# Kernel optimization log

Hardware: AMD Instinct MI355X
Metric: run time of the kernel (lower is better)

Reference implementation:

```python
import jax, jax.numpy as jnp
import numpy as np
from jax import lax

NEG_SLOPE = 0.2
BN_EPS = 1e-5


def _edges(n_nodes, n_total):
    # complete graph (no self loops) on the first n_nodes nodes, as in create_complete_graph,
    # plus PyG GATConv default add_self_loops over ALL n_total nodes.
    i = np.arange(n_nodes)
    src = np.repeat(i, n_nodes)
    dst = np.tile(i, n_nodes)
    keep = src != dst
    loops = np.arange(n_total)
    src = np.concatenate([src[keep], loops]).astype(np.int32)
    dst = np.concatenate([dst[keep], loops]).astype(np.int32)
    return jnp.asarray(src), jnp.asarray(dst)


def _bn_eval(x, g, b, m, v):
    # x: [B, C, H, W]; eval-mode batchnorm with running stats
    inv = g / jnp.sqrt(v + BN_EPS)
    return x * inv[None, :, None, None] + (b - m * inv)[None, :, None, None]


def _gat(x, W, a_src, a_dst, bias, src, dst, n_total):
    h = x @ W                      # [N, D_out]
    s = h @ a_src                  # [N] per-node source score
    d = h @ a_dst                  # [N] per-node dest score
    e = jax.nn.leaky_relu(s[src] + d[dst], NEG_SLOPE)          # [E]
    emax = jax.ops.segment_max(e, dst, num_segments=n_total)   # [N]
    ex = jnp.exp(e - emax[dst])
    denom = jax.ops.segment_sum(ex, dst, num_segments=n_total)
    alpha = ex / denom[dst]                                    # [E]
    out = jax.ops.segment_sum(alpha[:, None] * h[src], dst, num_segments=n_total)
    return out + bias


def setup_inputs() -> dict:
    key = jax.random.key(0)
    ks = jax.random.split(key, 12)
    B, H, W = 8, 64, 64

    def rn(k, shape, s):
        return jax.random.normal(k, shape, jnp.float32) * s

    return {
        "images": jax.random.normal(ks[0], (B, 3, H, W), jnp.float32),
        "conv1_w": rn(ks[1], (64, 3, 3, 3), 0.1), "conv1_b": jnp.zeros((64,), jnp.float32),
        "bn1_g": jnp.ones((64,), jnp.float32), "bn1_b": jnp.zeros((64,), jnp.float32),
        "bn1_m": jnp.zeros((64,), jnp.float32), "bn1_v": jnp.ones((64,), jnp.float32),
        "conv2_w": rn(ks[2], (128, 64, 3, 3), 0.05), "conv2_b": jnp.zeros((128,), jnp.float32),
        "bn2_g": jnp.ones((128,), jnp.float32), "bn2_b": jnp.zeros((128,), jnp.float32),
        "bn2_m": jnp.zeros((128,), jnp.float32), "bn2_v": jnp.ones((128,), jnp.float32),
        "gat1_w": rn(ks[3], (128, 256), 0.05), "gat1_asrc": rn(ks[4], (256,), 0.05),
        "gat1_adst": rn(ks[5], (256,), 0.05), "gat1_bias": jnp.zeros((256,), jnp.float32),
        "gat2_w": rn(ks[6], (256, 128), 0.05), "gat2_asrc": rn(ks[7], (128,), 0.05),
        "gat2_adst": rn(ks[8], (128,), 0.05), "gat2_bias": jnp.zeros((128,), jnp.float32),
        "out_w": rn(ks[9], (128, 10), 0.05), "out_b": jnp.zeros((10,), jnp.float32),
    }


def reference(images, conv1_w, conv1_b, bn1_g, bn1_b, bn1_m, bn1_v,
              conv2_w, conv2_b, bn2_g, bn2_b, bn2_m, bn2_v,
              gat1_w, gat1_asrc, gat1_adst, gat1_bias,
              gat2_w, gat2_asrc, gat2_adst, gat2_bias,
              out_w, out_b):
    dn = ("NCHW", "OIHW", "NCHW")
    x = lax.conv_general_dilated(images, conv1_w, (1, 1), "SAME", dimension_numbers=dn)
    x = x + conv1_b[None, :, None, None]
    x = jax.nn.relu(_bn_eval(x, bn1_g, bn1_b, bn1_m, bn1_v))
    x = lax.reduce_window(x, -jnp.inf, lax.max, (1, 1, 2, 2), (1, 1, 2, 2), "VALID")
    x = lax.conv_general_dilated(x, conv2_w, (1, 1), "SAME", dimension_numbers=dn)
    x = x + conv2_b[None, :, None, None]
    x = jax.nn.relu(_bn_eval(x, bn2_g, bn2_b, bn2_m, bn2_v))

    B = x.shape[0]
    n_nodes = x.shape[2] * x.shape[3]          # (H/2)*(W/2) = 1024
    x = x.reshape(B, 128, n_nodes).transpose(0, 2, 1).reshape(-1, 128)  # [B*n, 128]
    n_total = B * n_nodes
    src, dst = _edges(n_nodes, n_total)

    x = jax.nn.relu(_gat(x, gat1_w, gat1_asrc, gat1_adst, gat1_bias, src, dst, n_total))
    x = jax.nn.relu(_gat(x, gat2_w, gat2_asrc, gat2_adst, gat2_bias, src, dst, n_total))

    x = x.reshape(B, n_nodes, 128).mean(axis=1)   # global_mean_pool over each image's nodes
    logits = x @ out_w + out_b
    return jax.nn.log_softmax(logits, axis=1)
```

## Files before the change

kernel.cpp:

```cpp
#include <hip/hip_runtime.h>
#include <math.h>

#define BN_EPS 1e-5f
#define NEG_SLOPE 0.2f

__device__ __forceinline__ float relu_f(float x) { return x > 0.f ? x : 0.f; }
__device__ __forceinline__ float leaky_f(float z) { return z > 0.f ? z : NEG_SLOPE * z; }

__global__ void conv1_pool(const float* __restrict__ img, const float* __restrict__ w,
                           const float* __restrict__ cb, const float* __restrict__ g,
                           const float* __restrict__ bb, const float* __restrict__ m,
                           const float* __restrict__ vv, float* __restrict__ out)
{
    int blk = blockIdx.x;
    int q = blk & 3, cog = (blk >> 2) & 15, b = blk >> 6;
    int t = threadIdx.x;
    int x = t & 31, y = (q << 3) + (t >> 5);

    float acc[4][4] = {};
#pragma unroll
    for (int ci = 0; ci < 3; ++ci) {
        const float* ib = img + (b * 3 + ci) * 4096;
        float rv[4][4];
#pragma unroll
        for (int r = 0; r < 4; ++r) {
            int yy = 2 * y - 1 + r;
            bool yok = (unsigned)yy < 64u;
            const float* p = ib + yy * 64 + 2 * x;
            float2 c01 = yok ? *(const float2*)p : make_float2(0.f, 0.f);
            rv[r][1] = c01.x;
            rv[r][2] = c01.y;
            rv[r][0] = (yok && x > 0) ? p[-1] : 0.f;
            rv[r][3] = (yok && x < 31) ? p[2] : 0.f;
        }
#pragma unroll
        for (int j = 0; j < 4; ++j) {
            const float* wj = w + ((cog * 4 + j) * 3 + ci) * 9;
#pragma unroll
            for (int ky = 0; ky < 3; ++ky)
#pragma unroll
                for (int kx = 0; kx < 3; ++kx) {
                    float wvv = wj[ky * 3 + kx];
#pragma unroll
                    for (int py = 0; py < 2; ++py)
#pragma unroll
                        for (int px = 0; px < 2; ++px)
                            acc[j][py * 2 + px] += rv[py + ky][px + kx] * wvv;
                }
        }
    }
#pragma unroll
    for (int j = 0; j < 4; ++j) {
        int co = cog * 4 + j;
        float inv = g[co] / sqrtf(vv[co] + BN_EPS);
        float sh = cb[co] * inv + (bb[co] - m[co] * inv);
        float v0 = relu_f(acc[j][0] * inv + sh);
        float v1 = relu_f(acc[j][1] * inv + sh);
        float v2 = relu_f(acc[j][2] * inv + sh);
        float v3 = relu_f(acc[j][3] * inv + sh);
        out[((b * 64 + co) * 32 + y) * 32 + x] = fmaxf(fmaxf(v0, v1), fmaxf(v2, v3));
    }
}

__global__ void conv2_split(const float* __restrict__ in, const float* __restrict__ w,
                            float* __restrict__ pacc01, float* __restrict__ pacc23)
{
    int blk = blockIdx.x;
    int kz = blk & 3, half = (blk >> 2) & 1, cog = (blk >> 3) & 31, b = blk >> 8;
    int t = threadIdx.x;
    int x2p = (t & 15) * 2;
    int y = half * 16 + (t >> 4);
    bool xnz = x2p != 0;
    bool xhi = x2p == 30;
    const float* ibase = in + b * 64 * 1024 + kz * 16 * 1024;
    int xb = xnz ? x2p - 1 : 0;

    float acc[4][2] = {};

#pragma unroll 2
    for (int ci = 0; ci < 16; ++ci) {
        const float* cb2 = ibase + ci * 1024;
        float rc[3][4];
#pragma unroll
        for (int r = 0; r < 3; ++r) {
            int yy = y - 1 + r;
            bool yok = (unsigned)yy < 32u;
            const float* p = cb2 + yy * 32 + xb;
            float4 f = yok ? *(const float4*)p : make_float4(0.f, 0.f, 0.f, 0.f);
            rc[r][0] = xnz ? f.x : 0.f;
            rc[r][1] = xnz ? f.y : f.x;
            rc[r][2] = xnz ? f.z : f.y;
            float r3 = xnz ? f.w : f.z;
            rc[r][3] = xhi ? 0.f : r3;
        }
#pragma unroll
        for (int j = 0; j < 4; ++j) {
            const float* wj = w + ((cog * 4 + j) * 64 + kz * 16 + ci) * 9;
#pragma unroll
            for (int ky = 0; ky < 3; ++ky)
#pragma unroll
                for (int kx = 0; kx < 3; ++kx) {
                    float wvv = wj[ky * 3 + kx];
                    acc[j][0] += rc[ky][kx] * wvv;
                    acc[j][1] += rc[ky][kx + 1] * wvv;
                }
        }
    }

    float* pp = (kz & 2 ? pacc23 : pacc01) + (size_t)(kz & 1) * 1048576;
    int bid = b * 64 + cog * 2 + half;
    size_t base = ((size_t)bid * 256 + t) * 8;
    float4 s0 = {acc[0][0], acc[1][0], acc[2][0], acc[3][0]};
    float4 s1 = {acc[0][1], acc[1][1], acc[2][1], acc[3][1]};
    *(float4*)&pp[base] = s0;
    *(float4*)&pp[base + 4] = s1;
}

__global__ void conv2_combine(const float* __restrict__ p01, const float* __restrict__ p23,
                              const float* __restrict__ cb, const float* __restrict__ g,
                              const float* __restrict__ bb, const float* __restrict__ m,
                              const float* __restrict__ vv, float* __restrict__ x0)
{
    int gid = blockIdx.x * 256 + threadIdx.x;
    int t = gid & 255, bid = gid >> 8;
    int half = bid & 1, cog = (bid >> 1) & 31, b = bid >> 6;
    size_t off = (size_t)gid * 8;

    float4 s0 = {0.f, 0.f, 0.f, 0.f}, s1 = {0.f, 0.f, 0.f, 0.f};
    const float* pl0 = p01;
    const float* pl1 = p01 + 1048576;
    const float* pl2 = p23;
    const float* pl3 = p23 + 1048576;
#pragma unroll
    for (int kz = 0; kz < 4; ++kz) {
        const float* pp = kz == 0 ? pl0 : kz == 1 ? pl1 : kz == 2 ? pl2 : pl3;
        float4 u0 = *(const float4*)&pp[off];
        float4 u1 = *(const float4*)&pp[off + 4];
        s0.x += u0.x; s0.y += u0.y; s0.z += u0.z; s0.w += u0.w;
        s1.x += u1.x; s1.y += u1.y; s1.z += u1.z; s1.w += u1.w;
    }

    float4 gg = ((const float4*)g)[cog];
    float4 vvv = ((const float4*)vv)[cog];
    float4 bbb = ((const float4*)bb)[cog];
    float4 mm = ((const float4*)m)[cog];
    float4 cbb = ((const float4*)cb)[cog];
    float ix = gg.x / sqrtf(vvv.x + BN_EPS);
    float iy = gg.y / sqrtf(vvv.y + BN_EPS);
    float iz = gg.z / sqrtf(vvv.z + BN_EPS);
    float iw = gg.w / sqrtf(vvv.w + BN_EPS);
    float shx = cbb.x * ix + (bbb.x - mm.x * ix);
    float shy = cbb.y * iy + (bbb.y - mm.y * iy);
    float shz = cbb.z * iz + (bbb.z - mm.z * iz);
    float shw = cbb.w * iw + (bbb.w - mm.w * iw);

    float4 o0 = {relu_f(s0.x * ix + shx), relu_f(s0.y * iy + shy),
                 relu_f(s0.z * iz + shz), relu_f(s0.w * iw + shw)};
    float4 o1 = {relu_f(s1.x * ix + shx), relu_f(s1.y * iy + shy),
                 relu_f(s1.z * iz + shz), relu_f(s1.w * iw + shw)};

    int y = half * 16 + (t >> 4), x2p = (t & 15) * 2;
    int n0 = b * 1024 + y * 32 + x2p;
    *(float4*)&x0[(size_t)n0 * 128 + cog * 4] = o0;
    *(float4*)&x0[(size_t)(n0 + 1) * 128 + cog * 4] = o1;
}

template <int K, int N, bool SELF, bool SCORE>
__global__ void gemm32(const float* __restrict__ A, const float* __restrict__ Ahi,
                       const float* __restrict__ abias,
                       const float* __restrict__ B, float* __restrict__ C,
                       const float* __restrict__ asrc, const float* __restrict__ adst,
                       float* __restrict__ sp, float* __restrict__ dp)
{
    __shared__ float As[16][32];
    __shared__ float Bs[16][64];
    int t = threadIdx.x;
    int m0 = blockIdx.x * 32;
    int n0 = blockIdx.y * 64;
    int tx = t & 15, ty = t >> 4;
    int am = t >> 2, akq = (t & 3) * 4;
    bool hi = SELF && m0 >= 1024;
    const float* Ab = hi ? Ahi : A;
    float acc[4][4] = {};

    for (int k0 = 0; k0 < K; k0 += 16) {
        float4 av = *(const float4*)&Ab[(size_t)(m0 + am) * K + k0 + akq];
        if (hi) {
            float4 bz = *(const float4*)&abias[k0 + akq];
            av.x = relu_f(av.x + bz.x);
            av.y = relu_f(av.y + bz.y);
            av.z = relu_f(av.z + bz.z);
            av.w = relu_f(av.w + bz.w);
        }
        float4 bv0 = *(const float4*)&B[(size_t)(k0 + ty) * N + n0 + tx * 4];
        float4 bv1 = *(const float4*)&B[(size_t)(k0 + 8 + ty) * N + n0 + tx * 4];
        __syncthreads();
        As[akq + 0][am] = av.x;
        As[akq + 1][am] = av.y;
        As[akq + 2][am] = av.z;
        As[akq + 3][am] = av.w;
        *(float4*)&Bs[ty][tx * 4] = bv0;
        *(float4*)&Bs[ty + 8][tx * 4] = bv1;
        __syncthreads();
#pragma unroll
        for (int kk = 0; kk < 16; ++kk) {
            float4 a4 = *(const float4*)&As[kk][ty * 4];
            float4 b4 = *(const float4*)&Bs[kk][tx * 4];
            float aa[4] = {a4.x, a4.y, a4.z, a4.w};
            float bb4[4] = {b4.x, b4.y, b4.z, b4.w};
#pragma unroll
            for (int i = 0; i < 4; ++i)
#pragma unroll
                for (int j = 0; j < 4; ++j)
                    acc[i][j] += aa[i] * bb4[j];
        }
    }
#pragma unroll
    for (int i = 0; i < 4; ++i) {
        float4 o = {acc[i][0], acc[i][1], acc[i][2], acc[i][3]};
        *(float4*)&C[(size_t)(m0 + ty * 4 + i) * N + n0 + tx * 4] = o;
    }

    if (SCORE && m0 < 1024) {
        float4 as4 = *(const float4*)&asrc[n0 + tx * 4];
        float4 ad4 = *(const float4*)&adst[n0 + tx * 4];
#pragma unroll
        for (int i = 0; i < 4; ++i) {
            float ss = acc[i][0] * as4.x + acc[i][1] * as4.y +
                       acc[i][2] * as4.z + acc[i][3] * as4.w;
            float dd = acc[i][0] * ad4.x + acc[i][1] * ad4.y +
                       acc[i][2] * ad4.z + acc[i][3] * ad4.w;
#pragma unroll
            for (int off = 1; off < 16; off <<= 1) {
                ss += __shfl_xor(ss, off);
                dd += __shfl_xor(dd, off);
            }
            if (tx == 0) {
                sp[blockIdx.y * 1024 + m0 + ty * 4 + i] = ss;
                dp[blockIdx.y * 1024 + m0 + ty * 4 + i] = dd;
            }
        }
    }
}

template <int D, int KS, int NT>
__global__ void gat_agg_gemm(const float* __restrict__ h, const float* __restrict__ sp,
                             const float* __restrict__ dp, float* __restrict__ pacc,
                             float* __restrict__ pden)
{
    __shared__ float Ss[1024];
    __shared__ float As[16][32];
    __shared__ float Bs[16][64];
    __shared__ float red[2];
    __shared__ float part[16][32];

    const int CH = 1024 / KS;
    int t = threadIdx.x;
    int m0 = blockIdx.x * 32;
    int n0 = blockIdx.y * 64;
    int kz = blockIdx.z;
    int tx = t & 15, ty = t >> 4;
    int ug = t >> 3, vg4 = (t & 7) * 4;

    float4 sa = {0.f, 0.f, 0.f, 0.f}, sb = {0.f, 0.f, 0.f, 0.f};
#pragma unroll
    for (int nt = 0; nt < NT; ++nt) {
        float4 u = *(const float4*)&sp[nt * 1024 + t * 8];
        float4 v = *(const float4*)&sp[nt * 1024 + t * 8 + 4];
        sa.x += u.x; sa.y += u.y; sa.z += u.z; sa.w += u.w;
        sb.x += v.x; sb.y += v.y; sb.z += v.z; sb.w += v.w;
    }
    *(float4*)&Ss[t * 8] = sa;
    *(float4*)&Ss[t * 8 + 4] = sb;
    float lm = fmaxf(fmaxf(fmaxf(sa.x, sa.y), fmaxf(sa.z, sa.w)),
                     fmaxf(fmaxf(sb.x, sb.y), fmaxf(sb.z, sb.w)));
#pragma unroll
    for (int off = 1; off < 64; off <<= 1) lm = fmaxf(lm, __shfl_xor(lm, off));
    if ((t & 63) == 0) red[t >> 6] = lm;
    __syncthreads();
    float smax = fmaxf(red[0], red[1]);

    float4 dv = {0.f, 0.f, 0.f, 0.f};
#pragma unroll
    for (int nt = 0; nt < NT; ++nt) {
        float4 u = *(const float4*)&dp[nt * 1024 + m0 + vg4];
        dv.x += u.x; dv.y += u.y; dv.z += u.z; dv.w += u.w;
    }
    float4 mv = {leaky_f(smax + dv.x), leaky_f(smax + dv.y),
                 leaky_f(smax + dv.z), leaky_f(smax + dv.w)};
    float4 dsum = {0.f, 0.f, 0.f, 0.f};
    float acc[4][4] = {};

    for (int k0 = kz * CH; k0 < kz * CH + CH; k0 += 16) {
        float4 bv0 = *(const float4*)&h[(size_t)(k0 + ty) * D + n0 + tx * 4];
        float4 bv1 = *(const float4*)&h[(size_t)(k0 + 8 + ty) * D + n0 + tx * 4];
        float su = Ss[k0 + ug];
        float4 avv;
        avv.x = __expf(leaky_f(su + dv.x) - mv.x);
        avv.y = __expf(leaky_f(su + dv.y) - mv.y);
        avv.z = __expf(leaky_f(su + dv.z) - mv.z);
        avv.w = __expf(leaky_f(su + dv.w) - mv.w);
        dsum.x += avv.x; dsum.y += avv.y; dsum.z += avv.z; dsum.w += avv.w;
        __syncthreads();
        *(float4*)&As[ug][vg4] = avv;
        *(float4*)&Bs[ty][tx * 4] = bv0;
        *(float4*)&Bs[ty + 8][tx * 4] = bv1;
        __syncthreads();
#pragma unroll
        for (int kk = 0; kk < 16; ++kk) {
            float4 a4 = *(const float4*)&As[kk][ty * 4];
            float4 b4 = *(const float4*)&Bs[kk][tx * 4];
            float aa[4] = {a4.x, a4.y, a4.z, a4.w};
            float bb4[4] = {b4.x, b4.y, b4.z, b4.w};
#pragma unroll
            for (int i = 0; i < 4; ++i)
#pragma unroll
                for (int j = 0; j < 4; ++j)
                    acc[i][j] += aa[i] * bb4[j];
        }
    }

    __syncthreads();
    *(float4*)&part[ug][vg4] = dsum;
    __syncthreads();

#pragma unroll
    for (int i = 0; i < 4; ++i) {
        int r = ty * 4 + i;
        float4 o = {acc[i][0], acc[i][1], acc[i][2], acc[i][3]};
        *(float4*)&pacc[((size_t)kz * 1024 + m0 + r) * D + n0 + tx * 4] = o;
    }
    if (t < 32) {
        float den = 0.f;
#pragma unroll
        for (int u = 0; u < 16; ++u) den += part[u][t];
        pden[kz * 1024 + m0 + t] = den;
    }
}

template <int D, int KS>
__global__ void gat_combine(const float* __restrict__ pacc, const float* __restrict__ pden,
                            const float* __restrict__ bias, float* __restrict__ out)
{
    int idx = blockIdx.x * blockDim.x + threadIdx.x;
    if (idx >= 1024 * D / 4) return;
    int c4 = idx & (D / 4 - 1);
    int v = idx / (D / 4);
    float4 a = {0.f, 0.f, 0.f, 0.f};
    float den = 0.f;
#pragma unroll
    for (int ks = 0; ks < KS; ++ks) {
        float4 p = ((const float4*)pacc)[(size_t)(ks * 1024 + v) * (D / 4) + c4];
        a.x += p.x; a.y += p.y; a.z += p.z; a.w += p.w;
        den += pden[ks * 1024 + v];
    }
    float rd = 1.f / den;
    float4 bz = ((const float4*)bias)[c4];
    float4 o = {relu_f(a.x * rd + bz.x), relu_f(a.y * rd + bz.y),
                relu_f(a.z * rd + bz.z), relu_f(a.w * rd + bz.w)};
    ((float4*)out)[(size_t)v * (D / 4) + c4] = o;
}

__global__ void pool_part(const float* __restrict__ x2, const float* __restrict__ h2,
                          const float* __restrict__ bias2, float* __restrict__ part)
{
    int b = blockIdx.x >> 4, seg = blockIdx.x & 15, t = threadIdx.x;
    float acc = 0.f;
    if (b == 0) {
        const float* p = x2 + ((size_t)seg * 64) * 128 + t;
#pragma unroll 8
        for (int n = 0; n < 64; ++n) acc += p[(size_t)n * 128];
    } else {
        float bz = bias2[t];
        const float* p = h2 + ((size_t)b * 1024 + seg * 64) * 128 + t;
#pragma unroll 8
        for (int n = 0; n < 64; ++n) acc += relu_f(p[(size_t)n * 128] + bz);
    }
    part[(b * 16 + seg) * 128 + t] = acc;
}

__global__ void head_kernel(const float* __restrict__ part, const float* __restrict__ ow,
                            const float* __restrict__ ob, float* __restrict__ out)
{
    __shared__ float pooled[128];
    __shared__ float logits[10];
    int b = blockIdx.x, t = threadIdx.x;
    float acc = 0.f;
#pragma unroll
    for (int sgi = 0; sgi < 16; ++sgi) acc += part[(b * 16 + sgi) * 128 + t];
    pooled[t] = acc * (1.f / 1024.f);
    __syncthreads();
    if (t < 10) {
        float l = ob[t];
        for (int c = 0; c < 128; ++c) l += pooled[c] * ow[c * 10 + t];
        logits[t] = l;
    }
    __syncthreads();
    if (t == 0) {
        float mx = logits[0];
        for (int j = 1; j < 10; ++j) mx = fmaxf(mx, logits[j]);
        float sum = 0.f;
        for (int j = 0; j < 10; ++j) sum += expf(logits[j] - mx);
        float lse = mx + logf(sum);
        for (int j = 0; j < 10; ++j) out[b * 10 + j] = logits[j] - lse;
    }
}

extern "C" void kernel_launch(void* const* d_in, const int* in_sizes, int n_in,
                              void* d_out, int out_size, void* d_ws, size_t ws_size,
                              hipStream_t stream)
{
    const float* images = (const float*)d_in[0];
    const float* c1w = (const float*)d_in[1];
    const float* c1b = (const float*)d_in[2];
    const float* bn1g = (const float*)d_in[3];
    const float* bn1b = (const float*)d_in[4];
    const float* bn1m = (const float*)d_in[5];
    const float* bn1v = (const float*)d_in[6];
    const float* c2w = (const float*)d_in[7];
    const float* c2b = (const float*)d_in[8];
    const float* bn2g = (const float*)d_in[9];
    const float* bn2b = (const float*)d_in[10];
    const float* bn2m = (const float*)d_in[11];
    const float* bn2v = (const float*)d_in[12];
    const float* g1w = (const float*)d_in[13];
    const float* g1as = (const float*)d_in[14];
    const float* g1ad = (const float*)d_in[15];
    const float* g1b = (const float*)d_in[16];
    const float* g2w = (const float*)d_in[17];
    const float* g2as = (const float*)d_in[18];
    const float* g2ad = (const float*)d_in[19];
    const float* g2b = (const float*)d_in[20];
    const float* ow = (const float*)d_in[21];
    const float* ob = (const float*)d_in[22];
    float* out = (float*)d_out;

    float* ws = (float*)d_ws;
    float* x1    = ws;
    float* bufc1 = ws + 2097152;
    float* h1    = ws + 2621440;
    float* x0    = ws + 4718592;
    float* h2    = ws + 5767168;
    float* sp1   = ws + 6815744;
    float* dp1   = ws + 6819840;
    float* sp2   = ws + 6823936;
    float* dp2   = ws + 6825984;
    float* part  = bufc1;
    float* pden1 = bufc1 + 16384;
    float* pden2 = bufc1 + 24576;
    float* pacc1 = x0;
    float* pacc2 = h1;
    float* x2    = x0;
    float* c2p01 = x1;
    float* c2p23 = h1;

    conv1_pool<<<512, 256, 0, stream>>>(images, c1w, c1b, bn1g, bn1b, bn1m, bn1v, bufc1);
    conv2_split<<<2048, 256, 0, stream>>>(bufc1, c2w, c2p01, c2p23);
    conv2_combine<<<512, 256, 0, stream>>>(c2p01, c2p23, c2b, bn2g, bn2b, bn2m, bn2v, x0);

    gemm32<128, 256, false, true><<<dim3(256, 4), 128, 0, stream>>>(
        x0, x0, nullptr, g1w, h1, g1as, g1ad, sp1, dp1);
    gat_agg_gemm<256, 8, 4><<<dim3(32, 4, 8), 128, 0, stream>>>(h1, sp1, dp1, pacc1, pden1);
    gat_combine<256, 8><<<256, 256, 0, stream>>>(pacc1, pden1, g1b, x1);

    gemm32<256, 128, true, true><<<dim3(256, 2), 128, 0, stream>>>(
        x1, h1, g1b, g2w, h2, g2as, g2ad, sp2, dp2);
    gat_agg_gemm<128, 16, 2><<<dim3(32, 2, 16), 128, 0, stream>>>(h2, sp2, dp2, pacc2, pden2);
    gat_combine<128, 16><<<128, 256, 0, stream>>>(pacc2, pden2, g2b, x2);

    pool_part<<<128, 128, 0, stream>>>(x2, h2, g2b, part);
    head_kernel<<<8, 128, 0, stream>>>(part, ow, ob, out);
}
```

Baseline: 204.3 us.

## Halve conv2 K-split and use 256-thread GEMM/aggregation blocks with 2x4 microtiles

The conv2 input-channel split drops from 4 to 2 partial slices. This halves the partial-sum traffic and simplifies the combine step to two reads, at the cost of fewer blocks, each doing more serial work. The gemm32 and gat_agg_gemm kernels move from 128 threads with 4x4 per-thread tiles to 256 threads with 2x4 tiles, and the A smem tile is padded to 33 columns. This raises the thread count per block and lowers register pressure, but each thread now reuses fewer values from shared memory per load.

```diff
diff --git a/kernel.cpp b/kernel.cpp
--- a/kernel.cpp
+++ b/kernel.cpp
@@ -63,22 +63,22 @@
 }
 
 __global__ void conv2_split(const float* __restrict__ in, const float* __restrict__ w,
-                            float* __restrict__ pacc01, float* __restrict__ pacc23)
+                            float* __restrict__ c2p)
 {
     int blk = blockIdx.x;
-    int kz = blk & 3, half = (blk >> 2) & 1, cog = (blk >> 3) & 31, b = blk >> 8;
+    int kz = blk & 1, half = (blk >> 1) & 1, cog = (blk >> 2) & 31, b = blk >> 7;
     int t = threadIdx.x;
     int x2p = (t & 15) * 2;
     int y = half * 16 + (t >> 4);
     bool xnz = x2p != 0;
     bool xhi = x2p == 30;
-    const float* ibase = in + b * 64 * 1024 + kz * 16 * 1024;
+    const float* ibase = in + b * 65536 + kz * 32768;
     int xb = xnz ? x2p - 1 : 0;
 
     float acc[4][2] = {};
 
 #pragma unroll 2
-    for (int ci = 0; ci < 16; ++ci) {
+    for (int ci = 0; ci < 32; ++ci) {
         const float* cb2 = ibase + ci * 1024;
         float rc[3][4];
 #pragma unroll
@@ -95,7 +95,7 @@
         }
 #pragma unroll
         for (int j = 0; j < 4; ++j) {
-            const float* wj = w + ((cog * 4 + j) * 64 + kz * 16 + ci) * 9;
+            const float* wj = w + ((cog * 4 + j) * 64 + kz * 32 + ci) * 9;
 #pragma unroll
             for (int ky = 0; ky < 3; ++ky)
 #pragma unroll
@@ -107,7 +107,7 @@
         }
     }
 
-    float* pp = (kz & 2 ? pacc23 : pacc01) + (size_t)(kz & 1) * 1048576;
+    float* pp = c2p + (size_t)kz * 1048576;
     int bid = b * 64 + cog * 2 + half;
     size_t base = ((size_t)bid * 256 + t) * 8;
     float4 s0 = {acc[0][0], acc[1][0], acc[2][0], acc[3][0]};
@@ -116,7 +116,7 @@
     *(float4*)&pp[base + 4] = s1;
 }
 
-__global__ void conv2_combine(const float* __restrict__ p01, const float* __restrict__ p23,
+__global__ void conv2_combine(const float* __restrict__ c2p,
                               const float* __restrict__ cb, const float* __restrict__ g,
                               const float* __restrict__ bb, const float* __restrict__ m,
                               const float* __restrict__ vv, float* __restrict__ x0)
@@ -126,19 +126,12 @@
     int half = bid & 1, cog = (bid >> 1) & 31, b = bid >> 6;
     size_t off = (size_t)gid * 8;
 
-    float4 s0 = {0.f, 0.f, 0.f, 0.f}, s1 = {0.f, 0.f, 0.f, 0.f};
-    const float* pl0 = p01;
-    const float* pl1 = p01 + 1048576;
-    const float* pl2 = p23;
-    const float* pl3 = p23 + 1048576;
-#pragma unroll
-    for (int kz = 0; kz < 4; ++kz) {
-        const float* pp = kz == 0 ? pl0 : kz == 1 ? pl1 : kz == 2 ? pl2 : pl3;
-        float4 u0 = *(const float4*)&pp[off];
-        float4 u1 = *(const float4*)&pp[off + 4];
-        s0.x += u0.x; s0.y += u0.y; s0.z += u0.z; s0.w += u0.w;
-        s1.x += u1.x; s1.y += u1.y; s1.z += u1.z; s1.w += u1.w;
-    }
+    float4 u0 = *(const float4*)&c2p[off];
+    float4 u1 = *(const float4*)&c2p[off + 4];
+    float4 w0 = *(const float4*)&c2p[1048576 + off];
+    float4 w1 = *(const float4*)&c2p[1048576 + off + 4];
+    float sx = u0.x + w0.x, sy = u0.y + w0.y, sz = u0.z + w0.z, sw = u0.w + w0.w;
+    float qx = u1.x + w1.x, qy = u1.y + w1.y, qz = u1.z + w1.z, qw = u1.w + w1.w;
 
     float4 gg = ((const float4*)g)[cog];
     float4 vvv = ((const float4*)vv)[cog];
@@ -154,10 +147,10 @@
     float shz = cbb.z * iz + (bbb.z - mm.z * iz);
     float shw = cbb.w * iw + (bbb.w - mm.w * iw);
 
-    float4 o0 = {relu_f(s0.x * ix + shx), relu_f(s0.y * iy + shy),
-                 relu_f(s0.z * iz + shz), relu_f(s0.w * iw + shw)};
-    float4 o1 = {relu_f(s1.x * ix + shx), relu_f(s1.y * iy + shy),
-                 relu_f(s1.z * iz + shz), relu_f(s1.w * iw + shw)};
+    float4 o0 = {relu_f(sx * ix + shx), relu_f(sy * iy + shy),
+                 relu_f(sz * iz + shz), relu_f(sw * iw + shw)};
+    float4 o1 = {relu_f(qx * ix + shx), relu_f(qy * iy + shy),
+                 relu_f(qz * iz + shz), relu_f(qw * iw + shw)};
 
     int y = half * 16 + (t >> 4), x2p = (t & 15) * 2;
     int n0 = b * 1024 + y * 32 + x2p;
@@ -172,60 +165,50 @@
                        const float* __restrict__ asrc, const float* __restrict__ adst,
                        float* __restrict__ sp, float* __restrict__ dp)
 {
-    __shared__ float As[16][32];
+    __shared__ float As[16][33];
     __shared__ float Bs[16][64];
     int t = threadIdx.x;
     int m0 = blockIdx.x * 32;
     int n0 = blockIdx.y * 64;
     int tx = t & 15, ty = t >> 4;
-    int am = t >> 2, akq = (t & 3) * 4;
+    int am = t >> 3, ak2 = (t & 7) * 2;
     bool hi = SELF && m0 >= 1024;
     const float* Ab = hi ? Ahi : A;
-    float acc[4][4] = {};
+    float acc[2][4] = {};
 
     for (int k0 = 0; k0 < K; k0 += 16) {
-        float4 av = *(const float4*)&Ab[(size_t)(m0 + am) * K + k0 + akq];
+        float2 av = *(const float2*)&Ab[(size_t)(m0 + am) * K + k0 + ak2];
         if (hi) {
-            float4 bz = *(const float4*)&abias[k0 + akq];
-            av.x = relu_f(av.x + bz.x);
-            av.y = relu_f(av.y + bz.y);
-            av.z = relu_f(av.z + bz.z);
-            av.w = relu_f(av.w + bz.w);
-        }
-        float4 bv0 = *(const float4*)&B[(size_t)(k0 + ty) * N + n0 + tx * 4];
-        float4 bv1 = *(const float4*)&B[(size_t)(k0 + 8 + ty) * N + n0 + tx * 4];
+            av.x = relu_f(av.x + abias[k0 + ak2]);
+            av.y = relu_f(av.y + abias[k0 + ak2 + 1]);
+        }
+        float4 bv = *(const float4*)&B[(size_t)(k0 + ty) * N + n0 + tx * 4];
         __syncthreads();
-        As[akq + 0][am] = av.x;
-        As[akq + 1][am] = av.y;
-        As[akq + 2][am] = av.z;
-        As[akq + 3][am] = av.w;
-        *(float4*)&Bs[ty][tx * 4] = bv0;
-        *(float4*)&Bs[ty + 8][tx * 4] = bv1;
+        As[ak2][am] = av.x;
+        As[ak2 + 1][am] = av.y;
+        *(float4*)&Bs[ty][tx * 4] = bv;
         __syncthreads();
 #pragma unroll
         for (int kk = 0; kk < 16; ++kk) {
-            float4 a4 = *(const float4*)&As[kk][ty * 4];
+            float a0 = As[kk][ty * 2], a1 = As[kk][ty * 2 + 1];
             float4 b4 = *(const float4*)&Bs[kk][tx * 4];
-            float aa[4] = {a4.x, a4.y, a4.z, a4.w};
-            float bb4[4] = {b4.x, b4.y, b4.z, b4.w};
-#pragma unroll
-            for (int i = 0; i < 4; ++i)
-#pragma unroll
-                for (int j = 0; j < 4; ++j)
-                    acc[i][j] += aa[i] * bb4[j];
-        }
-    }
-#pragma unroll
-    for (int i = 0; i < 4; ++i) {
+            acc[0][0] += a0 * b4.x; acc[0][1] += a0 * b4.y;
+            acc[0][2] += a0 * b4.z; acc[0][3] += a0 * b4.w;
+            acc[1][0] += a1 * b4.x; acc[1][1] += a1 * b4.y;
+            acc[1][2] += a1 * b4.z; acc[1][3] += a1 * b4.w;
+        }
+    }
+#pragma unroll
+    for (int i = 0; i < 2; ++i) {
         float4 o = {acc[i][0], acc[i][1], acc[i][2], acc[i][3]};
-        *(float4*)&C[(size_t)(m0 + ty * 4 + i) * N + n0 + tx * 4] = o;
+        *(float4*)&C[(size_t)(m0 + ty * 2 + i) * N + n0 + tx * 4] = o;
     }
 
     if (SCORE && m0 < 1024) {
         float4 as4 = *(const float4*)&asrc[n0 + tx * 4];
         float4 ad4 = *(const float4*)&adst[n0 + tx * 4];
 #pragma unroll
-        for (int i = 0; i < 4; ++i) {
+        for (int i = 0; i < 2; ++i) {
             float ss = acc[i][0] * as4.x + acc[i][1] * as4.y +
                        acc[i][2] * as4.z + acc[i][3] * as4.w;
             float dd = acc[i][0] * ad4.x + acc[i][1] * ad4.y +
@@ -236,8 +219,8 @@
                 dd += __shfl_xor(dd, off);
             }
             if (tx == 0) {
-                sp[blockIdx.y * 1024 + m0 + ty * 4 + i] = ss;
-                dp[blockIdx.y * 1024 + m0 + ty * 4 + i] = dd;
+                sp[blockIdx.y * 1024 + m0 + ty * 2 + i] = ss;
+                dp[blockIdx.y * 1024 + m0 + ty * 2 + i] = dd;
             }
         }
     }
@@ -249,9 +232,9 @@
                              float* __restrict__ pden)
 {
     __shared__ float Ss[1024];
-    __shared__ float As[16][32];
+    __shared__ float As[16][33];
     __shared__ float Bs[16][64];
-    __shared__ float red[2];
+    __shared__ float red[4];
     __shared__ float part[16][32];
 
     const int CH = 1024 / KS;
@@ -260,75 +243,63 @@
     int n0 = blockIdx.y * 64;
     int kz = blockIdx.z;
     int tx = t & 15, ty = t >> 4;
-    int ug = t >> 3, vg4 = (t & 7) * 4;
-
-    float4 sa = {0.f, 0.f, 0.f, 0.f}, sb = {0.f, 0.f, 0.f, 0.f};
+    int vg2 = tx * 2;
+
+    float4 sa = {0.f, 0.f, 0.f, 0.f};
 #pragma unroll
     for (int nt = 0; nt < NT; ++nt) {
-        float4 u = *(const float4*)&sp[nt * 1024 + t * 8];
-        float4 v = *(const float4*)&sp[nt * 1024 + t * 8 + 4];
+        float4 u = *(const float4*)&sp[nt * 1024 + t * 4];
         sa.x += u.x; sa.y += u.y; sa.z += u.z; sa.w += u.w;
-        sb.x += v.x; sb.y += v.y; sb.z += v.z; sb.w += v.w;
-    }
-    *(float4*)&Ss[t * 8] = sa;
-    *(float4*)&Ss[t * 8 + 4] = sb;
-    float lm = fmaxf(fmaxf(fmaxf(sa.x, sa.y), fmaxf(sa.z, sa.w)),
-                     fmaxf(fmaxf(sb.x, sb.y), fmaxf(sb.z, sb.w)));
+    }
+    *(float4*)&Ss[t * 4] = sa;
+    float lm = fmaxf(fmaxf(sa.x, sa.y), fmaxf(sa.z, sa.w));
 #pragma unroll
     for (int off = 1; off < 64; off <<= 1) lm = fmaxf(lm, __shfl_xor(lm, off));
     if ((t & 63) == 0) red[t >> 6] = lm;
     __syncthreads();
-    float smax = fmaxf(red[0], red[1]);
-
-    float4 dv = {0.f, 0.f, 0.f, 0.f};
+    float smax = fmaxf(fmaxf(red[0], red[1]), fmaxf(red[2], red[3]));
+
+    float dv0 = 0.f, dv1 = 0.f;
 #pragma unroll
     for (int nt = 0; nt < NT; ++nt) {
-        float4 u = *(const float4*)&dp[nt * 1024 + m0 + vg4];
-        dv.x += u.x; dv.y += u.y; dv.z += u.z; dv.w += u.w;
-    }
-    float4 mv = {leaky_f(smax + dv.x), leaky_f(smax + dv.y),
-                 leaky_f(smax + dv.z), leaky_f(smax + dv.w)};
-    float4 dsum = {0.f, 0.f, 0.f, 0.f};
-    float acc[4][4] = {};
+        dv0 += dp[nt * 1024 + m0 + vg2];
+        dv1 += dp[nt * 1024 + m0 + vg2 + 1];
+    }
+    float mv0 = leaky_f(smax + dv0), mv1 = leaky_f(smax + dv1);
+    float ds0 = 0.f, ds1 = 0.f;
+    float acc[2][4] = {};
 
     for (int k0 = kz * CH; k0 < kz * CH + CH; k0 += 16) {
-        float4 bv0 = *(const float4*)&h[(size_t)(k0 + ty) * D + n0 + tx * 4];
-        float4 bv1 = *(const float4*)&h[(size_t)(k0 + 8 + ty) * D + n0 + tx * 4];
-        float su = Ss[k0 + ug];
-        float4 avv;
-        avv.x = __expf(leaky_f(su + dv.x) - mv.x);
-        avv.y = __expf(leaky_f(su + dv.y) - mv.y);
-        avv.z = __expf(leaky_f(su + dv.z) - mv.z);
-        avv.w = __expf(leaky_f(su + dv.w) - mv.w);
-        dsum.x += avv.x; dsum.y += avv.y; dsum.z += avv.z; dsum.w += avv.w;
+        float4 bv = *(const float4*)&h[(size_t)(k0 + ty) * D + n0 + tx * 4];
+        float su = Ss[k0 + ty];
+        float a0 = __expf(leaky_f(su + dv0) - mv0);
+        float a1 = __expf(leaky_f(su + dv1) - mv1);
+        ds0 += a0; ds1 += a1;
         __syncthreads();
-        *(float4*)&As[ug][vg4] = avv;
-        *(float4*)&Bs[ty][tx * 4] = bv0;
-        *(float4*)&Bs[ty + 8][tx * 4] = bv1;
+        As[ty][vg2] = a0;
+        As[ty][vg2 + 1] = a1;
+        *(float4*)&Bs[ty][tx * 4] = bv;
         __syncthreads();
 #pragma unroll
         for (int kk = 0; kk < 16; ++kk) {
-            float4 a4 = *(const float4*)&As[kk][ty * 4];
+            float a0m = As[kk][ty * 2], a1m = As[kk][ty * 2 + 1];
             float4 b4 = *(const float4*)&Bs[kk][tx * 4];
-            float aa[4] = {a4.x, a4.y, a4.z, a4.w};
-            float bb4[4] = {b4.x, b4.y, b4.z, b4.w};
-#pragma unroll
-            for (int i = 0; i < 4; ++i)
-#pragma unroll
-                for (int j = 0; j < 4; ++j)
-                    acc[i][j] += aa[i] * bb4[j];
+            acc[0][0] += a0m * b4.x; acc[0][1] += a0m * b4.y;
+            acc[0][2] += a0m * b4.z; acc[0][3] += a0m * b4.w;
+            acc[1][0] += a1m * b4.x; acc[1][1] += a1m * b4.y;
+            acc[1][2] += a1m * b4.z; acc[1][3] += a1m * b4.w;
         }
     }
 
     __syncthreads();
-    *(float4*)&part[ug][vg4] = dsum;
+    part[ty][vg2] = ds0;
+    part[ty][vg2 + 1] = ds1;
     __syncthreads();
 
 #pragma unroll
-    for (int i = 0; i < 4; ++i) {
-        int r = ty * 4 + i;
+    for (int i = 0; i < 2; ++i) {
         float4 o = {acc[i][0], acc[i][1], acc[i][2], acc[i][3]};
-        *(float4*)&pacc[((size_t)kz * 1024 + m0 + r) * D + n0 + tx * 4] = o;
+        *(float4*)&pacc[((size_t)kz * 1024 + m0 + ty * 2 + i) * D + n0 + tx * 4] = o;
     }
     if (t < 32) {
         float den = 0.f;
@@ -451,21 +422,20 @@
     float* pacc1 = x0;
     float* pacc2 = h1;
     float* x2    = x0;
-    float* c2p01 = x1;
-    float* c2p23 = h1;
+    float* c2p   = x1;
 
     conv1_pool<<<512, 256, 0, stream>>>(images, c1w, c1b, bn1g, bn1b, bn1m, bn1v, bufc1);
-    conv2_split<<<2048, 256, 0, stream>>>(bufc1, c2w, c2p01, c2p23);
-    conv2_combine<<<512, 256, 0, stream>>>(c2p01, c2p23, c2b, bn2g, bn2b, bn2m, bn2v, x0);
-
-    gemm32<128, 256, false, true><<<dim3(256, 4), 128, 0, stream>>>(
+    conv2_split<<<1024, 256, 0, stream>>>(bufc1, c2w, c2p);
+    conv2_combine<<<512, 256, 0, stream>>>(c2p, c2b, bn2g, bn2b, bn2m, bn2v, x0);
+
+    gemm32<128, 256, false, true><<<dim3(256, 4), 256, 0, stream>>>(
         x0, x0, nullptr, g1w, h1, g1as, g1ad, sp1, dp1);
-    gat_agg_gemm<256, 8, 4><<<dim3(32, 4, 8), 128, 0, stream>>>(h1, sp1, dp1, pacc1, pden1);
+    gat_agg_gemm<256, 8, 4><<<dim3(32, 4, 8), 256, 0, stream>>>(h1, sp1, dp1, pacc1, pden1);
     gat_combine<256, 8><<<256, 256, 0, stream>>>(pacc1, pden1, g1b, x1);
 
-    gemm32<256, 128, true, true><<<dim3(256, 2), 128, 0, stream>>>(
+    gemm32<256, 128, true, true><<<dim3(256, 2), 256, 0, stream>>>(
         x1, h1, g1b, g2w, h2, g2as, g2ad, sp2, dp2);
-    gat_agg_gemm<128, 16, 2><<<dim3(32, 2, 16), 128, 0, stream>>>(h2, sp2, dp2, pacc2, pden2);
+    gat_agg_gemm<128, 16, 2><<<dim3(32, 2, 16), 256, 0, stream>>>(h2, sp2, dp2, pacc2, pden2);
     gat_combine<128, 16><<<128, 256, 0, stream>>>(pacc2, pden2, g2b, x2);
 
     pool_part<<<128, 128, 0, stream>>>(x2, h2, g2b, part);
```

After: 205.3 us. About the same (+0.5%).
